# Kernel tuning notes

Hardware: AMD Instinct MI355X
Metric: run time of the kernel (lower is better)

Reference implementation:

```python
import jax, jax.numpy as jnp
import numpy as np

N_NODES = 10000
N_EDGES = 320000
IN_DIM = 64
HIDDEN = 128
HEADS = 4
OUT_DIM = 64
NEG_SLOPE = 0.2  # PyG GATConv default leaky_relu slope


def setup_inputs() -> dict:
    key = jax.random.key(0)
    ks = jax.random.split(key, 20)
    s = 0.05
    inp = {
        "x": jax.random.normal(ks[0], (N_NODES, IN_DIM), jnp.float32),
        "edge_index": jax.random.randint(ks[1], (2, N_EDGES), 0, N_NODES, jnp.int64),
        # GRU layer 0 (input IN_DIM -> HIDDEN), gates ordered [r, z, n] as in torch
        "w_ih0": jax.random.normal(ks[2], (3 * HIDDEN, IN_DIM), jnp.float32) * s,
        "w_hh0": jax.random.normal(ks[3], (3 * HIDDEN, HIDDEN), jnp.float32) * s,
        "b_ih0": jax.random.normal(ks[4], (3 * HIDDEN,), jnp.float32) * s,
        "b_hh0": jax.random.normal(ks[5], (3 * HIDDEN,), jnp.float32) * s,
        # GRU layer 1 (HIDDEN -> HIDDEN)
        "w_ih1": jax.random.normal(ks[6], (3 * HIDDEN, HIDDEN), jnp.float32) * s,
        "w_hh1": jax.random.normal(ks[7], (3 * HIDDEN, HIDDEN), jnp.float32) * s,
        "b_ih1": jax.random.normal(ks[8], (3 * HIDDEN,), jnp.float32) * s,
        "b_hh1": jax.random.normal(ks[9], (3 * HIDDEN,), jnp.float32) * s,
        # GAT layer 1: HIDDEN -> HIDDEN per head, HEADS heads, concat
        "W1": jax.random.normal(ks[10], (HIDDEN, HEADS * HIDDEN), jnp.float32) * s,
        "att_src1": jax.random.normal(ks[11], (HEADS, HIDDEN), jnp.float32) * s,
        "att_dst1": jax.random.normal(ks[12], (HEADS, HIDDEN), jnp.float32) * s,
        "bias1": jnp.zeros((HEADS * HIDDEN,), jnp.float32),
        # GAT layer 2: HEADS*HIDDEN -> OUT_DIM, 1 head
        "W2": jax.random.normal(ks[13], (HEADS * HIDDEN, OUT_DIM), jnp.float32) * s,
        "att_src2": jax.random.normal(ks[14], (1, OUT_DIM), jnp.float32) * s,
        "att_dst2": jax.random.normal(ks[15], (1, OUT_DIM), jnp.float32) * s,
        "bias2": jnp.zeros((OUT_DIM,), jnp.float32),
    }
    return inp


def _gru_layer(x, w_ih, w_hh, b_ih, b_hh):
    # x: [T, in]; torch GRU cell, unbatched, gates [r, z, n]
    H = w_hh.shape[1]
    gi = x @ w_ih.T + b_ih  # [T, 3H] precomputed input projections

    def step(h, gi_t):
        gh = h @ w_hh.T + b_hh
        i_r, i_z, i_n = jnp.split(gi_t, 3)
        h_r, h_z, h_n = jnp.split(gh, 3)
        r = jax.nn.sigmoid(i_r + h_r)
        z = jax.nn.sigmoid(i_z + h_z)
        n = jnp.tanh(i_n + r * h_n)
        h_new = (1.0 - z) * n + z * h
        return h_new, h_new

    h0 = jnp.zeros((H,), x.dtype)
    _, out = jax.lax.scan(step, h0, gi)
    return out  # [T, H]


def _gat(x, src, dst, W, att_src, att_dst, bias):
    # PyG GATConv (eval mode, add_self_loops=True, concat=True)
    N = x.shape[0]
    heads, C = att_src.shape
    h = (x @ W).reshape(N, heads, C)  # [N, H, C]
    loop = jnp.arange(N, dtype=src.dtype)
    s = jnp.concatenate([src, loop])
    d = jnp.concatenate([dst, loop])
    a_s = jnp.einsum("nhc,hc->nh", h, att_src)  # [N, H]
    a_d = jnp.einsum("nhc,hc->nh", h, att_dst)
    e = jax.nn.leaky_relu(a_s[s] + a_d[d], NEG_SLOPE)  # [E, H]
    m = jax.ops.segment_max(e, d, num_segments=N)  # per-dst max (every node has self loop)
    ex = jnp.exp(e - m[d])
    denom = jax.ops.segment_sum(ex, d, num_segments=N)
    alpha = ex / denom[d]  # [E, H]
    out = jax.ops.segment_sum(alpha[:, :, None] * h[s], d, num_segments=N)  # [N, H, C]
    return out.reshape(N, heads * C) + bias


def reference(x, edge_index,
              w_ih0, w_hh0, b_ih0, b_hh0,
              w_ih1, w_hh1, b_ih1, b_hh1,
              W1, att_src1, att_dst1, bias1,
              W2, att_src2, att_dst2, bias2):
    h = _gru_layer(x, w_ih0, w_hh0, b_ih0, b_hh0)
    h = _gru_layer(h, w_ih1, w_hh1, b_ih1, b_hh1)
    src, dst = edge_index[0], edge_index[1]
    h = _gat(h, src, dst, W1, att_src1, att_dst1, bias1)
    h = jax.nn.relu(h)
    out = _gat(h, src, dst, W2, att_src2, att_dst2, bias2)
    return out  # [N, OUT_DIM]
```

## Files before the change

kernel.cpp:

```cpp
#include <hip/hip_runtime.h>
#include <math.h>

#define NN_  10000
#define NE_  320000
#define IND  64
#define HID  128
#define G3   384
#define HC1  512
#define OUTD 64

#define CSR_CNT_BLKS 40
#define CSR_FILL_BLKS 40

typedef _Float16 h2f __attribute__((ext_vector_type(2)));
union UH4 { uint4 u; h2f h[4]; };

__device__ __forceinline__ float leakyf_(float x){ return x>0.f ? x : 0.2f*x; }
__device__ __forceinline__ float fsig_(float x){ return 1.f/(1.f+__expf(-x)); }
__device__ __forceinline__ float ftanh_(float x){ float e=__expf(2.f*x); return 1.f-2.f/(e+1.f); }

#define BARRIER_LDS() asm volatile("s_waitcnt lgkmcnt(0)\n\ts_barrier" ::: "memory")
#define WAIT_VM0()    asm volatile("s_waitcnt vmcnt(0)" ::: "memory")

__device__ __forceinline__ float ld_agent(const float* p) {
  return __hip_atomic_load(p, __ATOMIC_RELAXED, __HIP_MEMORY_SCOPE_AGENT);
}
__device__ __forceinline__ void st_agent(float* p, float v) {
  __hip_atomic_store(p, v, __ATOMIC_RELAXED, __HIP_MEMORY_SCOPE_AGENT);
}
__device__ __forceinline__ unsigned ld_agent_u32(const unsigned* p) {
  return __hip_atomic_load(p, __ATOMIC_RELAXED, __HIP_MEMORY_SCOPE_AGENT);
}
__device__ __forceinline__ void st_agent_u32(unsigned* p, unsigned v) {
  __hip_atomic_store(p, v, __ATOMIC_RELAXED, __HIP_MEMORY_SCOPE_AGENT);
}
__device__ __forceinline__ int ld_ctr(const int* p) {
  return __hip_atomic_load(p, __ATOMIC_ACQUIRE, __HIP_MEMORY_SCOPE_AGENT);
}
__device__ __forceinline__ void st_ctr(int* p, int v) {
  __hip_atomic_store(p, v, __ATOMIC_RELEASE, __HIP_MEMORY_SCOPE_AGENT);
}

template<bool TB>
__global__ __launch_bounds__(256) void gemm_k(const float* __restrict__ A,
                                              const float* __restrict__ B,
                                              const float* __restrict__ bias,
                                              float* __restrict__ C,
                                              int M, int N, int K,
                                              const float* __restrict__ att_src,
                                              const float* __restrict__ att_dst,
                                              float* a_s, float* a_d,
                                              int heads, int Catt) {
  __shared__ float As[16][65];
  __shared__ float Bs[16][65];
  __shared__ float sred[64];
  __shared__ float dred[64];
  const int bm = blockIdx.x * 64, bn = blockIdx.y * 64;
  const int tid = threadIdx.x;
  const int tm = (tid >> 4) << 2, tn = (tid & 15) << 2;
  float acc[4][4] = {};
  const int row = tid & 63, kq = (tid >> 6) << 2;
  for (int k0 = 0; k0 < K; k0 += 16) {
    float4 av = make_float4(0.f, 0.f, 0.f, 0.f);
    const int m = bm + row;
    if (m < M) av = *(const float4*)(A + (size_t)m * K + k0 + kq);
    As[kq + 0][row] = av.x; As[kq + 1][row] = av.y;
    As[kq + 2][row] = av.z; As[kq + 3][row] = av.w;
    if (TB) {
      float4 bv = *(const float4*)(B + (size_t)(bn + row) * K + k0 + kq);
      Bs[kq + 0][row] = bv.x; Bs[kq + 1][row] = bv.y;
      Bs[kq + 2][row] = bv.z; Bs[kq + 3][row] = bv.w;
    } else {
      const int kr = tid >> 4, nq = (tid & 15) << 2;
      float4 bv = *(const float4*)(B + (size_t)(k0 + kr) * N + bn + nq);
      Bs[kr][nq + 0] = bv.x; Bs[kr][nq + 1] = bv.y;
      Bs[kr][nq + 2] = bv.z; Bs[kr][nq + 3] = bv.w;
    }
    __syncthreads();
#pragma unroll
    for (int kk = 0; kk < 16; kk++) {
      float a[4], b[4];
#pragma unroll
      for (int i = 0; i < 4; i++) a[i] = As[kk][tm + i];
#pragma unroll
      for (int j = 0; j < 4; j++) b[j] = Bs[kk][tn + j];
#pragma unroll
      for (int i = 0; i < 4; i++)
#pragma unroll
        for (int j = 0; j < 4; j++) acc[i][j] = fmaf(a[i], b[j], acc[i][j]);
    }
    __syncthreads();
  }
#pragma unroll
  for (int i = 0; i < 4; i++) {
    const int m = bm + tm + i;
    if (m < M) {
#pragma unroll
      for (int j = 0; j < 4; j++) {
        const int n = bn + tn + j;
        float v = acc[i][j];
        if (bias) v += bias[n];
        C[(size_t)m * N + n] = v;
      }
    }
  }
  if (att_src) {
    if (tid < 64) { sred[tid] = 0.f; dred[tid] = 0.f; }
    __syncthreads();
    const int h = bn / Catt;
    const int cbase = bn + tn - h * Catt;
#pragma unroll
    for (int i = 0; i < 4; i++) {
      float ps = 0.f, pd = 0.f;
#pragma unroll
      for (int j = 0; j < 4; j++) {
        const float sa = att_src[h * Catt + cbase + j];
        const float da = att_dst[h * Catt + cbase + j];
        ps = fmaf(acc[i][j], sa, ps);
        pd = fmaf(acc[i][j], da, pd);
      }
      atomicAdd(&sred[tm + i], ps);
      atomicAdd(&dred[tm + i], pd);
    }
    __syncthreads();
    if (tid < 64) {
      const int m = bm + tid;
      if (m < M) {
        atomicAdd(&a_s[m * heads + h], sred[tid]);
        atomicAdd(&a_d[m * heads + h], dred[tid]);
      }
    }
  }
}

__global__ __launch_bounds__(256, 1) void gru_pipe(const float* __restrict__ gi0,
                                                   const float* __restrict__ w_hh0,
                                                   const float* __restrict__ b_hh0,
                                                   const float* __restrict__ w_ih1,
                                                   const float* __restrict__ b_ih1,
                                                   const float* __restrict__ w_hh1,
                                                   const float* __restrict__ b_hh1,
                                                   unsigned* h0_st16, float* gi1_st,
                                                   int* ctr,
                                                   float* __restrict__ h1_out,
                                                   int T,
                                                   const int* __restrict__ ei,
                                                   int* cnt, int* offs,
                                                   int* cursor, int* csr, int E) {
  __shared__ _Float16 hbuf[2][HID];
  __shared__ float psum[3][HID];
  __shared__ int sbuf[256];
  __shared__ int scarry;

  const int bid   = blockIdx.x;
  const int tid   = threadIdx.x;

  if (bid >= 4) {
    const int cb = bid - 4;
    if (cb < CSR_CNT_BLKS) {
      for (int e = cb * 256 + tid; e < E; e += CSR_CNT_BLKS * 256)
        atomicAdd(&cnt[ei[E + e]], 1);
      __syncthreads();
      if (tid == 0)
        __hip_atomic_fetch_add(&ctr[3], 1, __ATOMIC_RELEASE, __HIP_MEMORY_SCOPE_AGENT);
    } else if (cb == CSR_CNT_BLKS) {
      if (tid == 0) {
        while (ld_ctr(&ctr[3]) < CSR_CNT_BLKS) __builtin_amdgcn_s_sleep(32);
      }
      __syncthreads();
      if (tid == 0) scarry = 0;
      __syncthreads();
      for (int base = 0; base < NN_; base += 256) {
        const int i = base + tid;
        const int v = (i < NN_) ? cnt[i] : 0;
        sbuf[tid] = v;
        __syncthreads();
        for (int d = 1; d < 256; d <<= 1) {
          int t2 = 0;
          if (tid >= d) t2 = sbuf[tid - d];
          __syncthreads();
          sbuf[tid] += t2;
          __syncthreads();
        }
        const int incl = sbuf[tid] + scarry;
        if (i < NN_) { offs[i] = incl - v; cursor[i] = incl - v; }
        __syncthreads();
        if (tid == 255) scarry = incl;
        __syncthreads();
      }
      if (tid == 0) {
        offs[NN_] = scarry;
        __threadfence();
        st_ctr(&ctr[4], 1);
      }
    } else {
      const int fb = cb - CSR_CNT_BLKS - 1;
      if (tid == 0) {
        while (ld_ctr(&ctr[4]) < 1) __builtin_amdgcn_s_sleep(64);
      }
      __syncthreads();
      for (int e = fb * 256 + tid; e < E; e += CSR_FILL_BLKS * 256) {
        const int d = ei[E + e];
        const int s = ei[e];
        const int pos = atomicAdd(&cursor[d], 1);
        csr[pos] = s;
      }
    }
    return;
  }

  const int khalf = (tid >> 6) & 1;
  const int j     = (tid & 63) | ((tid >> 7) << 6);
  const int kbase = khalf * 64;

  const float* wsrc = (bid == 0) ? w_hh0 : (bid == 3 ? w_hh1 : w_ih1);
  const float* bsrc = (bid == 0) ? b_hh0 : (bid == 3 ? b_hh1 : b_ih1);

  h2f wr[32], wz[32], wn[32];
#pragma unroll
  for (int i = 0; i < 16; i++) {
    float4 a = *(const float4*)(wsrc + (size_t)j * HID + kbase + i * 4);
    wr[2 * i]     = h2f{(_Float16)a.x, (_Float16)a.y};
    wr[2 * i + 1] = h2f{(_Float16)a.z, (_Float16)a.w};
  }
#pragma unroll
  for (int i = 0; i < 16; i++) {
    float4 a = *(const float4*)(wsrc + (size_t)(j + HID) * HID + kbase + i * 4);
    wz[2 * i]     = h2f{(_Float16)a.x, (_Float16)a.y};
    wz[2 * i + 1] = h2f{(_Float16)a.z, (_Float16)a.w};
  }
#pragma unroll
  for (int i = 0; i < 16; i++) {
    float4 a = *(const float4*)(wsrc + (size_t)(j + 2 * HID) * HID + kbase + i * 4);
    wn[2 * i]     = h2f{(_Float16)a.x, (_Float16)a.y};
    wn[2 * i + 1] = h2f{(_Float16)a.z, (_Float16)a.w};
  }
  const float b0 = bsrc[j];
  const float b1 = bsrc[j + HID];
  const float b2 = bsrc[j + 2 * HID];

  auto dot_half = [&](const _Float16* hp16, float& r, float& z, float& n) {
    const uint4* hp = (const uint4*)(hp16 + kbase);
    float ar0 = 0.f, ar1 = 0.f, az0 = 0.f, az1 = 0.f, an0 = 0.f, an1 = 0.f;
#pragma unroll
    for (int c = 0; c < 2; c++) {
      uint4 hv[4];
#pragma unroll
      for (int i = 0; i < 4; i++) hv[i] = hp[c * 4 + i];
#pragma unroll
      for (int i = 0; i < 4; i++) {
        UH4 v; v.u = hv[i];
#pragma unroll
        for (int q = 0; q < 4; q++) {
          const int k = c * 16 + i * 4 + q;
          const h2f hh = v.h[q];
          if (k & 1) {
            ar1 = __builtin_amdgcn_fdot2(wr[k], hh, ar1, false);
            az1 = __builtin_amdgcn_fdot2(wz[k], hh, az1, false);
            an1 = __builtin_amdgcn_fdot2(wn[k], hh, an1, false);
          } else {
            ar0 = __builtin_amdgcn_fdot2(wr[k], hh, ar0, false);
            az0 = __builtin_amdgcn_fdot2(wz[k], hh, az0, false);
            an0 = __builtin_amdgcn_fdot2(wn[k], hh, an0, false);
          }
        }
      }
    }
    r = ar0 + ar1; z = az0 + az1; n = an0 + an1;
  };

  if (bid == 0 || bid == 3) {
    const float* gsrc = (bid == 0) ? gi0 : gi1_st;
    float hcur = 0.f;
    if (khalf == 0) hbuf[0][j] = (_Float16)0.f;
    BARRIER_LDS();

    if (bid == 3 && tid == 0) {
      while (ld_ctr(&ctr[1]) < 4) {}
      while (ld_ctr(&ctr[2]) < 4) {}
    }
    if (bid == 3) __syncthreads();

    float gxA, gyA, gzA, gxB, gyB, gzB, gxC, gyC, gzC, gxD, gyD, gzD;
    if (khalf == 0) {
      const float* gp = gsrc + j;
      gxA = gp[0]; gyA = gp[HID]; gzA = gp[2 * HID];
      gp = gsrc + (size_t)1 * G3 + j;
      gxB = gp[0]; gyB = gp[HID]; gzB = gp[2 * HID];
      gp = gsrc + (size_t)2 * G3 + j;
      gxC = gp[0]; gyC = gp[HID]; gzC = gp[2 * HID];
      gp = gsrc + (size_t)3 * G3 + j;
      gxD = gp[0]; gyD = gp[HID]; gzD = gp[2 * HID];
    }

    auto substep = [&](int tc, int pin, float& gx, float& gy, float& gz) {
      float dr, dz, dn;
      dot_half(&hbuf[pin][0], dr, dz, dn);
      if (khalf == 1) { psum[0][j] = dr; psum[1][j] = dz; psum[2][j] = dn; }
      BARRIER_LDS();
      if (khalf == 0) {
        const float r = fsig_(gx + b0 + dr + psum[0][j]);
        const float z = fsig_(gy + b1 + dz + psum[1][j]);
        const float n = ftanh_(gz + r * (b2 + dn + psum[2][j]));
        hcur = (1.f - z) * n + z * hcur;
        hbuf[pin ^ 1][j] = (_Float16)hcur;
        if (bid == 3) h1_out[(size_t)tc * HID + j] = hcur;
        const int tp = (tc + 4 < T) ? (tc + 4) : 0;
        const float* gp = gsrc + (size_t)tp * G3 + j;
        gx = gp[0]; gy = gp[HID]; gz = gp[2 * HID];
      }
      if (bid == 3 && tid == 0 && (tc & 31) == 0) {
        int need = tc + 36; if (need > T) need = T;
        while (ld_ctr(&ctr[1]) < need) {}
        while (ld_ctr(&ctr[2]) < need) {}
      }
      BARRIER_LDS();
      if (bid == 0 && tid >= 64 && tid < 128) {
        const int idx = tid - 64;
        unsigned v = *(const unsigned*)&hbuf[pin ^ 1][2 * idx];
        st_agent_u32(&h0_st16[(size_t)tc * 64 + idx], v);
        if ((tc & 15) == 15) {
          WAIT_VM0();
          if (tid == 64) st_ctr(&ctr[0], tc + 1);
        }
      }
    };

    for (int t = 0; t < T; t += 4) {
      substep(t,     0, gxA, gyA, gzA);
      substep(t + 1, 1, gxB, gyB, gzB);
      substep(t + 2, 0, gxC, gyC, gzC);
      substep(t + 3, 1, gxD, gyD, gzD);
    }
    if (bid == 0 && tid >= 64 && tid < 128) {
      WAIT_VM0();
      if (tid == 64) st_ctr(&ctr[0], T);
    }
  } else {
    const int f = bid - 1;
    _Float16* hstage = &hbuf[0][0];
    for (int t0 = f; t0 < T; t0 += 8) {
      if (tid == 0) {
        int need = t0 + 7; if (need > T) need = T;
        while (ld_ctr(&ctr[0]) < need) {}
      }
      __syncthreads();
      unsigned hv0 = 0, hv1 = 0, hv2 = 0, hv3 = 0;
      if (tid < 64) {
        hv0 = ld_agent_u32(&h0_st16[(size_t)t0 * 64 + tid]);
        if (t0 + 2 < T) hv1 = ld_agent_u32(&h0_st16[(size_t)(t0 + 2) * 64 + tid]);
        if (t0 + 4 < T) hv2 = ld_agent_u32(&h0_st16[(size_t)(t0 + 4) * 64 + tid]);
        if (t0 + 6 < T) hv3 = ld_agent_u32(&h0_st16[(size_t)(t0 + 6) * 64 + tid]);
      }
#pragma unroll
      for (int k = 0; k < 4; k++) {
        const int t = t0 + 2 * k;
        if (t >= T) break;
        if (tid < 64) {
          const unsigned hv = (k == 0) ? hv0 : (k == 1) ? hv1 : (k == 2) ? hv2 : hv3;
          ((unsigned*)hstage)[tid] = hv;
        }
        BARRIER_LDS();
        float dr, dz, dn;
        dot_half(hstage, dr, dz, dn);
        if (khalf == 1) { psum[0][j] = dr; psum[1][j] = dz; psum[2][j] = dn; }
        BARRIER_LDS();
        if (khalf == 0) {
          float* gp = gi1_st + (size_t)t * G3 + j;
          st_agent(gp,           dr + psum[0][j] + b0);
          st_agent(gp + HID,     dz + psum[1][j] + b1);
          st_agent(gp + 2 * HID, dn + psum[2][j] + b2);
        }
      }
      __syncthreads();
      if (tid == 0) {
        int pub = t0 + 8; if (pub > T) pub = T;
        st_ctr(&ctr[1 + f], pub);
      }
    }
    __syncthreads();
    if (tid == 0) st_ctr(&ctr[1 + f], T);
  }
}

__global__ void gat_agg(const float* __restrict__ feat,
                        const float* __restrict__ a_s, const float* __restrict__ a_d,
                        const int* __restrict__ offs, const int* __restrict__ csr,
                        const float* __restrict__ bias, float* __restrict__ out,
                        int heads, int cshift, int do_relu) {
  const int n = blockIdx.x;
  const int t = threadIdx.x;
  const int HC = blockDim.x;
  const int h = t >> cshift;
  const int beg = offs[n], end = offs[n + 1];
  const float ad = a_d[n * heads + h];
  const float self_e = leakyf_(a_s[n * heads + h] + ad);
  float m = self_e;
  for (int i = beg; i < end; i++) {
    const int s = csr[i];
    m = fmaxf(m, leakyf_(a_s[s * heads + h] + ad));
  }
  float den = expf(self_e - m);
  float acc = den * feat[(size_t)n * HC + t];
  for (int i = beg; i < end; i++) {
    const int s = csr[i];
    const float wgt = expf(leakyf_(a_s[s * heads + h] + ad) - m);
    den += wgt;
    acc = fmaf(wgt, feat[(size_t)s * HC + t], acc);
  }
  float o = acc / den + bias[t];
  if (do_relu) o = fmaxf(o, 0.f);
  out[(size_t)n * HC + t] = o;
}

extern "C" void kernel_launch(void* const* d_in, const int* in_sizes, int n_in,
                              void* d_out, int out_size, void* d_ws, size_t ws_size,
                              hipStream_t stream) {
  const float* x        = (const float*)d_in[0];
  const int*   ei       = (const int*)d_in[1];
  const float* w_ih0    = (const float*)d_in[2];
  const float* w_hh0    = (const float*)d_in[3];
  const float* b_ih0    = (const float*)d_in[4];
  const float* b_hh0    = (const float*)d_in[5];
  const float* w_ih1    = (const float*)d_in[6];
  const float* w_hh1    = (const float*)d_in[7];
  const float* b_ih1    = (const float*)d_in[8];
  const float* b_hh1    = (const float*)d_in[9];
  const float* W1       = (const float*)d_in[10];
  const float* att_src1 = (const float*)d_in[11];
  const float* att_dst1 = (const float*)d_in[12];
  const float* bias1    = (const float*)d_in[13];
  const float* W2       = (const float*)d_in[14];
  const float* att_src2 = (const float*)d_in[15];
  const float* att_dst2 = (const float*)d_in[16];
  const float* bias2    = (const float*)d_in[17];
  float* out = (float*)d_out;

  const int N = NN_;
  const int E = in_sizes[1] / 2;

  float* f    = (float*)d_ws;
  float* gi   = f;
  float* hmm1 = f;
  float* h1   = f + (size_t)N * HC1;
  float* g1o  = h1 + (size_t)N * HID;
  float* hmm2 = g1o + (size_t)N * HC1;
  float* as1  = hmm2 + (size_t)N * OUTD;
  float* ad1  = as1 + (size_t)N * 4;
  float* as2  = ad1 + (size_t)N * 4;
  float* ad2  = as2 + (size_t)N;
  int* cnt    = (int*)(ad2 + (size_t)N);
  int* offs   = cnt + N;
  int* cursor = offs + (N + 1);
  int* csr    = cursor + N;
  int* ctr    = csr + E;
  unsigned* h0_st16 = (unsigned*)g1o;
  float*    gi1_st  = g1o + (size_t)N * 64;

  const int mblocks = (N + 63) / 64;

  gemm_k<true><<<dim3(mblocks, G3 / 64), 256, 0, stream>>>(
      x, w_ih0, b_ih0, gi, N, G3, IND, nullptr, nullptr, nullptr, nullptr, 0, 0);
  hipMemsetAsync(ctr, 0, 6 * sizeof(int), stream);
  hipMemsetAsync(cnt, 0, (size_t)N * sizeof(int), stream);
  hipMemsetAsync(as1, 0, (size_t)N * 10 * sizeof(float), stream);
  gru_pipe<<<4 + CSR_CNT_BLKS + 1 + CSR_FILL_BLKS, 256, 0, stream>>>(
      gi, w_hh0, b_hh0, w_ih1, b_ih1, w_hh1, b_hh1,
      h0_st16, gi1_st, ctr, h1, N, ei, cnt, offs, cursor, csr, E);

  gemm_k<false><<<dim3(mblocks, HC1 / 64), 256, 0, stream>>>(
      h1, W1, nullptr, hmm1, N, HC1, HID, att_src1, att_dst1, as1, ad1, 4, HID);
  gat_agg<<<N, HC1, 0, stream>>>(hmm1, as1, ad1, offs, csr, bias1, g1o, 4, 7, 1);

  gemm_k<false><<<dim3(mblocks, OUTD / 64), 256, 0, stream>>>(
      g1o, W2, nullptr, hmm2, N, OUTD, HC1, att_src2, att_dst2, as2, ad2, 1, OUTD);
  gat_agg<<<N, OUTD, 0, stream>>>(hmm2, as2, ad2, offs, csr, bias2, out, 1, 6, 0);
}
```

Baseline: 6.050 ms.

## Stage GAT edge scores in LDS and use online softmax in aggregation

The GAT aggregation kernel now loads a chunk of neighbor indices cooperatively, with one edge per thread within each head. Each edge's attention logit is computed once into shared memory instead of being recomputed redundantly by every channel thread across two passes. An online-softmax rescale merges the max pass and the accumulate pass, so each edge chunk is read only once. This adds several block barriers per chunk and uses the fast __expf instead of expf.

```diff
diff --git a/kernel.cpp b/kernel.cpp
--- a/kernel.cpp
+++ b/kernel.cpp
@@ -388,25 +388,45 @@
                         const int* __restrict__ offs, const int* __restrict__ csr,
                         const float* __restrict__ bias, float* __restrict__ out,
                         int heads, int cshift, int do_relu) {
+  __shared__ float ech[512];
+  __shared__ int scs[128];
   const int n = blockIdx.x;
   const int t = threadIdx.x;
   const int HC = blockDim.x;
   const int h = t >> cshift;
+  const int C = 1 << cshift;
+  const int c = t & (C - 1);
   const int beg = offs[n], end = offs[n + 1];
   const float ad = a_d[n * heads + h];
-  const float self_e = leakyf_(a_s[n * heads + h] + ad);
-  float m = self_e;
-  for (int i = beg; i < end; i++) {
-    const int s = csr[i];
-    m = fmaxf(m, leakyf_(a_s[s * heads + h] + ad));
-  }
-  float den = expf(self_e - m);
-  float acc = den * feat[(size_t)n * HC + t];
-  for (int i = beg; i < end; i++) {
-    const int s = csr[i];
-    const float wgt = expf(leakyf_(a_s[s * heads + h] + ad) - m);
-    den += wgt;
-    acc = fmaf(wgt, feat[(size_t)s * HC + t], acc);
+  float m = leakyf_(a_s[n * heads + h] + ad);
+  float den = 1.f;
+  float acc = feat[(size_t)n * HC + t];
+  for (int base = beg; base < end; base += C) {
+    const int cnt = min(C, end - base);
+    float ev = 0.f;
+    if (c < cnt) {
+      const int sv = csr[base + c];
+      if (h == 0) scs[c] = sv;
+      ev = leakyf_(a_s[sv * heads + h] + ad);
+      ech[h * C + c] = ev;
+    }
+    __syncthreads();
+    float mc = m;
+    for (int i = 0; i < cnt; i++) mc = fmaxf(mc, ech[h * C + i]);
+    if (mc > m) {
+      const float sc = __expf(m - mc);
+      den *= sc; acc *= sc; m = mc;
+    }
+    __syncthreads();
+    if (c < cnt) ech[h * C + c] = __expf(ev - mc);
+    __syncthreads();
+    for (int i = 0; i < cnt; i++) {
+      const float al = ech[h * C + i];
+      const int s = scs[i];
+      den += al;
+      acc = fmaf(al, feat[(size_t)s * HC + t], acc);
+    }
+    __syncthreads();
   }
   float o = acc / den + bias[t];
   if (do_relu) o = fmaxf(o, 0.f);
```

Result: faster. 5.901 ms (-2.5%).
